# Kernel optimization log

Hardware: AMD Instinct MI355X
Metric: run time of the kernel (lower is better)

The kernel has to match this reference:

```python
import jax, jax.numpy as jnp
import numpy as np

B, N, D, C, ND = 32, 196, 512, 500, 51  # batch, patches, embed dim, classes, 1+50 descriptions


def _l2norm(x):
    return x / jnp.linalg.norm(x, axis=-1, keepdims=True)


def setup_inputs() -> dict:
    key = jax.random.key(0)
    k1, k2, k3, k4 = jax.random.split(key, 4)
    all_text = _l2norm(jax.random.normal(k3, (ND, C, D), jnp.float32))
    return {
        "image_features": _l2norm(jax.random.normal(k1, (B, D), jnp.float32)),
        "local_image_features": _l2norm(jax.random.normal(k2, (B, N, D), jnp.float32)),
        "all_text_features": all_text,
        "mean_text_features": _l2norm(jnp.mean(all_text, axis=0)),
        "topk": 50,
    }


def reference(image_features, local_image_features, all_text_features, mean_text_features, topk):
    # Faithful translation of get_dense_logits2 (m==1 global-feature axis squeezed out).
    base_logits = image_features @ mean_text_features.T                       # [B, C]
    # w[b,n] = <global image feat b, local patch feat n>
    w = jnp.einsum('bd,bnd->bn', image_features, local_image_features)        # [B, N]
    # v[nd,c]: softmax over descriptions of <mean text c, description nd of class c>
    v = jax.nn.softmax(
        jnp.einsum('cd,ncd->nc', mean_text_features, all_text_features), axis=0)  # [ND, C]
    # sim[b,c,nd,m] = <patch m of image b, description nd of class c>
    sim = jnp.einsum('bmd,ncd->bcnm', local_image_features, all_text_features)    # [B, C, ND, N]
    vals, idx = jax.lax.top_k(sim, topk)                                      # [B, C, ND, k] over patch axis
    sim_top = jnp.swapaxes(vals, 2, 3)                                        # [B, C, k, ND]
    # torch: idx[:, 0, :, 0] -> class 0, description 0, all k indices
    sel = idx[:, 0, 0, :]                                                     # [B, k]
    wg = jax.nn.softmax(jnp.take_along_axis(w, sel, axis=1), axis=-1)         # [B, k]
    # weight[b,c,m,n] = wg[b,m] * v[n,c]
    weight = wg[:, None, :, None] * jnp.swapaxes(v, 0, 1)[None, :, None, :]   # [B, C, k, ND]
    bias_logits = jnp.sum(sim_top * weight, axis=(-2, -1))                    # [B, C]
    return base_logits + bias_logits
```

## Files before the change

kernel.cpp:

```cpp
#include <hip/hip_runtime.h>

#define B_ 32
#define N_ 196
#define D_ 512
#define C_ 500
#define ND_ 51

typedef __attribute__((ext_vector_type(8))) short short8_t;
typedef __attribute__((ext_vector_type(4))) unsigned short us4_t;
typedef __attribute__((ext_vector_type(4))) float f32x4;

typedef const __attribute__((address_space(1))) unsigned int* gas_p;
typedef __attribute__((address_space(3))) unsigned int* las_p;
#define GLDS(gp, lp) __builtin_amdgcn_global_load_lds((gas_p)(gp), (las_p)(lp), 16, 0, 0)

__device__ inline unsigned short f2bf(float f) {
    unsigned u = __float_as_uint(f);
    u += 0x7FFFu + ((u >> 16) & 1u);
    return (unsigned short)(u >> 16);
}

template <int CTRL>
__device__ inline float dpp_mov(float x) {
    return __uint_as_float(__builtin_amdgcn_update_dpp(
        __float_as_uint(x), __float_as_uint(x), CTRL, 0xF, 0xF, true));
}
__device__ inline float rsum64(float v) {
    v += dpp_mov<0x121>(v);
    v += dpp_mov<0x122>(v);
    v += dpp_mov<0x124>(v);
    v += dpp_mov<0x128>(v);
    v += __shfl_xor(v, 16);
    v += __shfl_xor(v, 32);
    return v;
}
__device__ inline float rmax64(float v) {
    v = fmaxf(v, dpp_mov<0x121>(v));
    v = fmaxf(v, dpp_mov<0x122>(v));
    v = fmaxf(v, dpp_mov<0x124>(v));
    v = fmaxf(v, dpp_mov<0x128>(v));
    v = fmaxf(v, __shfl_xor(v, 16));
    v = fmaxf(v, __shfl_xor(v, 32));
    return v;
}
__device__ inline float rmin64(float v) {
    v = fminf(v, dpp_mov<0x121>(v));
    v = fminf(v, dpp_mov<0x122>(v));
    v = fminf(v, dpp_mov<0x124>(v));
    v = fminf(v, dpp_mov<0x128>(v));
    v = fminf(v, __shfl_xor(v, 16));
    v = fminf(v, __shfl_xor(v, 32));
    return v;
}
template <int S>
__device__ inline float xsh(float y) {
    if constexpr (S == 1) return dpp_mov<0xB1>(y);
    else if constexpr (S == 2) return dpp_mov<0x4E>(y);
    else if constexpr (S == 8) return dpp_mov<0x128>(y);
    else return __shfl_xor(y, S);
}

__global__ __launch_bounds__(256) void k_ctd(const float* __restrict__ text,
                                             const float* __restrict__ mean,
                                             unsigned short* __restrict__ textbf,
                                             float* __restrict__ dots) {
    const int row = blockIdx.x * 4 + (threadIdx.x >> 6);
    const int lane = threadIdx.x & 63;
    const int n = row / C_;
    const int ccol = row - n * C_;
    const float* tp = text + (size_t)row * 512 + lane * 8;
    const float* mp = mean + (size_t)ccol * 512 + lane * 8;
    const float4 f0 = *(const float4*)tp;
    const float4 f1 = *(const float4*)(tp + 4);
    const float4 m0 = *(const float4*)mp;
    const float4 m1 = *(const float4*)(mp + 4);
    float a = f0.x * m0.x + f0.y * m0.y + f0.z * m0.z + f0.w * m0.w
            + f1.x * m1.x + f1.y * m1.y + f1.z * m1.z + f1.w * m1.w;
    a = rsum64(a);
    const us4_t p0 = {f2bf(f0.x), f2bf(f0.y), f2bf(f0.z), f2bf(f0.w)};
    const us4_t p1 = {f2bf(f1.x), f2bf(f1.y), f2bf(f1.z), f2bf(f1.w)};
    *(us4_t*)&textbf[(size_t)row * 512 + lane * 8] = p0;
    *(us4_t*)&textbf[(size_t)row * 512 + lane * 8 + 4] = p1;
    if (lane == 0) dots[row] = a;
}

__global__ __launch_bounds__(64) void k_vsm(const float* __restrict__ dots,
                                            float* __restrict__ vout) {
    const int c = blockIdx.x;
    const int lane = threadIdx.x;
    float xv = (lane < ND_) ? dots[lane * C_ + c] : -INFINITY;
    float mx = rmax64(xv);
    float e = (lane < ND_) ? expf(xv - mx) : 0.f;
    float sum = rsum64(e);
    if (lane < ND_) vout[lane * C_ + c] = e / sum;
}

__global__ __launch_bounds__(256) void k_cls(const float* __restrict__ image,
                                             const float* __restrict__ localf,
                                             const float* __restrict__ text,
                                             unsigned short* __restrict__ localbf,
                                             float* __restrict__ s_ws,
                                             float* __restrict__ wm_ws) {
    const int row = blockIdx.x * 4 + (threadIdx.x >> 6);
    const int lane = threadIdx.x & 63;
    const int b = row / N_;
    const float* lp = localf + (size_t)row * 512 + lane * 8;
    const float4 l0 = *(const float4*)lp;
    const float4 l1 = *(const float4*)(lp + 4);
    const float* ip = image + b * 512 + lane * 8;
    const float* t0p = text + lane * 8;
    const float4 i0 = *(const float4*)ip, i1 = *(const float4*)(ip + 4);
    const float4 t0 = *(const float4*)t0p, t1 = *(const float4*)(t0p + 4);
    float a = l0.x * t0.x + l0.y * t0.y + l0.z * t0.z + l0.w * t0.w
            + l1.x * t1.x + l1.y * t1.y + l1.z * t1.z + l1.w * t1.w;
    float g = l0.x * i0.x + l0.y * i0.y + l0.z * i0.z + l0.w * i0.w
            + l1.x * i1.x + l1.y * i1.y + l1.z * i1.z + l1.w * i1.w;
    a = rsum64(a);
    g = rsum64(g);
    const us4_t p0 = {f2bf(l0.x), f2bf(l0.y), f2bf(l0.z), f2bf(l0.w)};
    const us4_t p1 = {f2bf(l1.x), f2bf(l1.y), f2bf(l1.z), f2bf(l1.w)};
    *(us4_t*)&localbf[(size_t)row * 512 + lane * 8] = p0;
    *(us4_t*)&localbf[(size_t)row * 512 + lane * 8 + 4] = p1;
    if (lane == 0) { s_ws[row] = a; wm_ws[row] = g; }
}

__global__ __launch_bounds__(256) void k_v(const float* __restrict__ mean,
                                           const float* __restrict__ text,
                                           float* __restrict__ vout) {
    const int c = blockIdx.x;
    const int w = threadIdx.x >> 6, lane = threadIdx.x & 63;
    __shared__ float sc[ND_];
    float md[8];
#pragma unroll
    for (int t = 0; t < 8; ++t) md[t] = mean[c * 512 + lane + 64 * t];
    for (int j = 0; j < 13; ++j) {
        const int n = w + 4 * j;
        if (n < ND_) {
            const float* tp = &text[((size_t)n * C_ + c) * 512];
            float a = 0.f;
#pragma unroll
            for (int t = 0; t < 8; ++t) a += md[t] * tp[lane + 64 * t];
            a = rsum64(a);
            if (lane == 0) sc[n] = a;
        }
    }
    __syncthreads();
    if (w == 0) {
        float xv = (lane < ND_) ? sc[lane] : -INFINITY;
        float mx = rmax64(xv);
        float e = (lane < ND_) ? expf(xv - mx) : 0.f;
        float sum = rsum64(e);
        if (lane < ND_) vout[lane * C_ + c] = e / sum;
    }
}

__global__ __launch_bounds__(256) void k_sw(const float* __restrict__ image,
                                            const float* __restrict__ localf,
                                            const float* __restrict__ text,
                                            float* __restrict__ s_ws,
                                            float* __restrict__ wm_ws) {
    const int b = blockIdx.x;
    const int m0 = blockIdx.y * 28;
    const int w = threadIdx.x >> 6, lane = threadIdx.x & 63;
    float t00[8], img[8];
#pragma unroll
    for (int t = 0; t < 8; ++t) {
        t00[t] = text[lane + 64 * t];
        img[t] = image[b * 512 + lane + 64 * t];
    }
    for (int t7 = 0; t7 < 7; ++t7) {
        const int m = m0 + w * 7 + t7;
        const float* lp = &localf[((size_t)b * N_ + m) * 512];
        float a = 0.f, g = 0.f;
#pragma unroll
        for (int t = 0; t < 8; ++t) {
            const float lv = lp[lane + 64 * t];
            a += t00[t] * lv;
            g += img[t] * lv;
        }
        a = rsum64(a);
        g = rsum64(g);
        if (lane == 0) { s_ws[b * N_ + m] = a; wm_ws[b * N_ + m] = g; }
    }
}

__global__ __launch_bounds__(64) void k_sel(const float* __restrict__ s_ws,
                                            const float* __restrict__ wm_ws,
                                            float* __restrict__ wgout) {
    const int b = blockIdx.x;
    const int lane = threadIdx.x;
    const unsigned long long ltmask = (1ull << lane) - 1ull;
    __shared__ float cv[64], cw[64];

    float x[4], p[4];
#pragma unroll
    for (int i = 0; i < 4; ++i) {
        const int m = lane + 64 * i;
        x[i] = (m < N_) ? s_ws[b * N_ + m] : -INFINITY;
        p[i] = (m < N_) ? wm_ws[b * N_ + m] : 0.f;
    }
    float lo = -1.02f, hi = 1.02f;
    int cl = N_;
    for (int it = 0; it < 24; ++it) {
        const float t = 0.5f * (lo + hi);
        int cnum = 0;
#pragma unroll
        for (int i = 0; i < 4; ++i) cnum += __popcll(__ballot(x[i] > t));
        if (cnum >= 50) { lo = t; cl = cnum; if (cnum <= 64) break; }
        else hi = t;
    }
    bool f[4];
    if (cl <= 64) {
#pragma unroll
        for (int i = 0; i < 4; ++i) f[i] = x[i] > lo;
    } else {
        int s1 = 0;
#pragma unroll
        for (int i = 0; i < 4; ++i) s1 += __popcll(__ballot(x[i] > hi));
        const int need = 64 - s1;
        int run = 0;
#pragma unroll
        for (int i = 0; i < 4; ++i) {
            const bool mid = (x[i] > lo) && !(x[i] > hi);
            const unsigned long long bm = __ballot(mid);
            const int pos = run + __popcll(bm & ltmask);
            f[i] = (x[i] > hi) || (mid && pos < need);
            run += __popcll(bm);
        }
    }
    int basep = 0;
#pragma unroll
    for (int i = 0; i < 4; ++i) {
        const unsigned long long bm = __ballot(f[i]);
        const int pos = basep + __popcll(bm & ltmask);
        if (f[i]) { cv[pos] = x[i]; cw[pos] = p[i]; }
        basep += __popcll(bm);
    }
    __builtin_amdgcn_s_waitcnt(0);
    float y = (lane < basep) ? cv[lane] : -INFINITY;
    float z = (lane < basep) ? cw[lane] : 0.f;
#pragma unroll
    for (int k = 2; k <= 64; k <<= 1) {
#pragma unroll
        for (int s2 = k >> 1; s2 > 0; s2 >>= 1) {
            const float py = __shfl_xor(y, s2);
            const float pz = __shfl_xor(z, s2);
            const bool keep_max = ((lane & k) == 0) == ((lane & s2) == 0);
            const bool take = keep_max ? (py > y) : (py < y);
            if (take) { y = py; z = pz; }
        }
    }
    float xv = (lane < 50) ? z : -INFINITY;
    float mx = xv;
#pragma unroll
    for (int off = 32; off; off >>= 1) mx = fmaxf(mx, __shfl_xor(mx, off));
    float e = (lane < 50) ? expf(xv - mx) : 0.f;
    float sum = e;
#pragma unroll
    for (int off = 32; off; off >>= 1) sum += __shfl_xor(sum, off);
    if (lane < 50) wgout[b * 50 + lane] = e / sum;
}

#define BSTEP(S, UP) { \
    const float q1 = xsh<S>(y1); \
    const float q2 = xsh<S>(y2); \
    if ((q1 > y1) == (UP)) y1 = q1; \
    if ((q2 > y2) == (UP)) y2 = q2; }

__global__ __launch_bounds__(512, 6) void k_main(const float* __restrict__ image,
                                                 const float* __restrict__ mean,
                                                 const unsigned short* __restrict__ localbf,
                                                 const unsigned short* __restrict__ textbf,
                                                 const float* __restrict__ vws,
                                                 const float* __restrict__ wgws,
                                                 float* __restrict__ out) {
    const int b = blockIdx.x;
    const int c = blockIdx.y;
    const int tid = threadIdx.x;
    const int w = tid >> 6;
    const int lane = tid & 63;
    const int quad = lane >> 4;
    const int l16 = lane & 15;

    __shared__ __align__(16) union SU {
        unsigned short stg[ND_ * 196 * 2];
        float ST[ND_ * 196];
    } u;

    float base_reg = 0.f;
    if (w == 0) {
        float s = 0.f;
#pragma unroll
        for (int t = 0; t < 8; ++t)
            s += image[b * 512 + lane + 64 * t] * mean[c * 512 + lane + 64 * t];
        s = rsum64(s);
        base_reg = s;
    }

    f32x4 acc[2][4];
    const f32x4 zv = {0.f, 0.f, 0.f, 0.f};
#pragma unroll
    for (int i = 0; i < 2; ++i)
#pragma unroll
        for (int j = 0; j < 4; ++j) acc[i][j] = zv;

    const unsigned short* abase = localbf + (size_t)(b * N_) * 512;

    const char* sp = (const char*)u.stg;
    const unsigned fb0 = (unsigned)(l16 * 128 + ((quad ^ (l16 & 7)) * 16));
    const unsigned fb1 = fb0 ^ 64u;
    const unsigned ab0 = fb0 + (unsigned)(w * 2048);
    const unsigned ab1 = fb1 + (unsigned)(w * 2048);

    for (int ks = 0; ks < 8; ++ks) {
#pragma unroll
        for (int i = 0; i < 4; ++i) {
            const int s = i * 512 + tid;
            if (s < 1568) {
                const int r = s >> 3;
                const int c8 = (s & 7) ^ (r & 7);
                GLDS(abase + (size_t)r * 512 + ks * 64 + c8 * 8, (char*)u.stg + s * 16);
            }
        }
        {
            const int s = tid;
            if (s < 408) {
                const int r = s >> 3;
                const int c8 = (s & 7) ^ (r & 7);
                GLDS(textbf + (size_t)(r * C_ + c) * 512 + ks * 64 + c8 * 8,
                     (char*)u.stg + 25088 + s * 16);
            }
        }
        __syncthreads();
#pragma unroll
        for (int kc = 0; kc < 2; ++kc) {
            const unsigned bb = kc ? fb1 : fb0;
            const unsigned aa = kc ? ab1 : ab0;
            short8_t bfr[4];
#pragma unroll
            for (int nt = 0; nt < 4; ++nt)
                bfr[nt] = *(const short8_t*)(sp + 25088 + bb + nt * 2048);
#pragma unroll
            for (int mi = 0; mi < 2; ++mi) {
                const int mt = w + 8 * mi;
                if (mt < 13) {
                    const short8_t af = *(const short8_t*)(sp + aa + mi * 16384);
#pragma unroll
                    for (int nt = 0; nt < 4; ++nt)
                        acc[mi][nt] = __builtin_amdgcn_mfma_f32_16x16x32_bf16(af, bfr[nt], acc[mi][nt], 0, 0, 0);
                }
            }
        }
        __syncthreads();
    }

#pragma unroll
    for (int nt = 0; nt < 4; ++nt) {
        const int n = nt * 16 + l16;
        if (n < ND_) {
#pragma unroll
            for (int mi = 0; mi < 2; ++mi) {
                const int mt = w + 8 * mi;
                if (mt < 12 || (mt == 12 && quad == 0))
                    *(f32x4*)&u.ST[n * 196 + mt * 16 + quad * 4] = acc[mi][nt];
            }
        }
    }
    __syncthreads();

    const float wgv = (lane < 50) ? wgws[b * 50 + lane] : 0.f;
    const unsigned long long ltmask = (1ull << lane) - 1ull;
    float waveacc = 0.f;

    const bool L0 = (lane & 1) == 0, L1 = (lane & 2) == 0, L2 = (lane & 4) == 0,
               L3 = (lane & 8) == 0, L4 = (lane & 16) == 0, L5 = (lane & 32) == 0;

    for (int t = 0; t < 4; ++t) {
        const int n1 = w + 16 * t;
        const int n2 = n1 + 8;
        const bool a2 = (n2 < ND_);
        if (n1 >= ND_) break;
        float* rowp1 = &u.ST[n1 * 196];
        float* rowp2 = &u.ST[(a2 ? n2 : n1) * 196];

        float x1[4], x2[4];
        float mn1 = INFINITY, mx1 = -INFINITY, mn2 = INFINITY, mx2 = -INFINITY;
        if (lane < 49) {
            f32x4 v1 = *(const f32x4*)&rowp1[lane * 4];
            f32x4 v2 = *(const f32x4*)&rowp2[lane * 4];
#pragma unroll
            for (int r = 0; r < 4; ++r) {
                x1[r] = v1[r];
                x2[r] = a2 ? v2[r] : -INFINITY;
                mx1 = fmaxf(mx1, x1[r]); mn1 = fminf(mn1, x1[r]);
                mx2 = fmaxf(mx2, x2[r]); mn2 = fminf(mn2, x2[r]);
            }
        } else {
#pragma unroll
            for (int r = 0; r < 4; ++r) { x1[r] = -INFINITY; x2[r] = -INFINITY; }
        }

        float hi1 = rmax64(mx1), lo1 = rmin64(mn1);
        float hi2 = rmax64(mx2), lo2 = rmin64(mn2);
        int cl1 = 256, cl2 = a2 ? 256 : 0;
        bool d1 = false, d2 = !a2;
        for (int it = 0; it < 24 && !(d1 && d2); ++it) {
            const float t1 = 0.5f * (lo1 + hi1);
            const float t2 = 0.5f * (lo2 + hi2);
            int cn1 = 0, cn2 = 0;
#pragma unroll
            for (int i = 0; i < 4; ++i) {
                cn1 += __popcll(__ballot(x1[i] > t1));
                cn2 += __popcll(__ballot(x2[i] > t2));
            }
            if (!d1) { if (cn1 >= 50) { lo1 = t1; cl1 = cn1; d1 = (cn1 <= 64); } else hi1 = t1; }
            if (!d2) { if (cn2 >= 50) { lo2 = t2; cl2 = cn2; d2 = (cn2 <= 64); } else hi2 = t2; }
        }

        bool f1[4], f2[4];
        int cnt1, cnt2;
        if (cl1 <= 64) {
#pragma unroll
            for (int i = 0; i < 4; ++i) f1[i] = x1[i] > lo1;
            cnt1 = cl1;
        } else {
            int s1 = 0;
#pragma unroll
            for (int i = 0; i < 4; ++i) s1 += __popcll(__ballot(x1[i] > hi1));
            const int need = 64 - s1;
            int run = 0;
#pragma unroll
            for (int i = 0; i < 4; ++i) {
                const bool mid = (x1[i] > lo1) && !(x1[i] > hi1);
                const unsigned long long bm = __ballot(mid);
                const int pos = run + __popcll(bm & ltmask);
                f1[i] = (x1[i] > hi1) || (mid && pos < need);
                run += __popcll(bm);
            }
            cnt1 = 64;
        }
        if (cl2 <= 64) {
#pragma unroll
            for (int i = 0; i < 4; ++i) f2[i] = x2[i] > lo2;
            cnt2 = cl2;
        } else {
            int s1 = 0;
#pragma unroll
            for (int i = 0; i < 4; ++i) s1 += __popcll(__ballot(x2[i] > hi2));
            const int need = 64 - s1;
            int run = 0;
#pragma unroll
            for (int i = 0; i < 4; ++i) {
                const bool mid = (x2[i] > lo2) && !(x2[i] > hi2);
                const unsigned long long bm = __ballot(mid);
                const int pos = run + __popcll(bm & ltmask);
                f2[i] = (x2[i] > hi2) || (mid && pos < need);
                run += __popcll(bm);
            }
            cnt2 = 64;
        }

        int bp1 = 0, bp2 = 0;
#pragma unroll
        for (int i = 0; i < 4; ++i) {
            const unsigned long long bm1 = __ballot(f1[i]);
            const unsigned long long bm2 = __ballot(f2[i]);
            const int p1 = bp1 + __popcll(bm1 & ltmask);
            const int p2 = bp2 + __popcll(bm2 & ltmask);
            if (f1[i]) rowp1[p1] = x1[i];
            if (f2[i]) rowp2[p2] = x2[i];
            bp1 += __popcll(bm1);
            bp2 += __popcll(bm2);
        }
        __builtin_amdgcn_s_waitcnt(0);
        float y1 = (lane < cnt1) ? rowp1[lane] : -INFINITY;
        float y2 = (lane < cnt2) ? rowp2[lane] : -INFINITY;

        BSTEP(1, L1 == L0)
        BSTEP(2, L2 == L1) BSTEP(1, L2 == L0)
        BSTEP(4, L3 == L2) BSTEP(2, L3 == L1) BSTEP(1, L3 == L0)
        BSTEP(8, L4 == L3) BSTEP(4, L4 == L2) BSTEP(2, L4 == L1) BSTEP(1, L4 == L0)
        BSTEP(16, L5 == L4) BSTEP(8, L5 == L3) BSTEP(4, L5 == L2) BSTEP(2, L5 == L1) BSTEP(1, L5 == L0)
        BSTEP(32, L5) BSTEP(16, L4) BSTEP(8, L3) BSTEP(4, L2) BSTEP(2, L1) BSTEP(1, L0)

        float part1 = (lane < 50) ? y1 * wgv : 0.f;
        float part2 = (lane < 50) ? y2 * wgv : 0.f;
        part1 = rsum64(part1);
        part2 = rsum64(part2);
        waveacc += vws[n1 * C_ + c] * part1;
        if (a2) waveacc += vws[n2 * C_ + c] * part2;
    }

    if (lane == 0) u.ST[w * 196] = waveacc;
    __syncthreads();
    if (tid == 0) {
        float r = base_reg;
#pragma unroll
        for (int i = 0; i < 8; ++i) r += u.ST[i * 196];
        out[b * C_ + c] = r;
    }
}

__global__ __launch_bounds__(256) void k_main_fb(const float* __restrict__ image,
                                                 const float* __restrict__ localf,
                                                 const float* __restrict__ text,
                                                 const float* __restrict__ mean,
                                                 const float* __restrict__ vws,
                                                 const float* __restrict__ wgws,
                                                 float* __restrict__ out) {
    const int c = blockIdx.x;
    const int b = blockIdx.y;
    const int tid = threadIdx.x;
    const int w = tid >> 6;
    const int lane = tid & 63;
    const int quad = lane >> 4;
    const int l16 = lane & 15;

    __shared__ __align__(16) union SU {
        struct { unsigned short A[208 * 72]; unsigned short Bm[64 * 72]; } st;
        float S[208 * 65];
    } u;
    __shared__ float wavepart[4];
    __shared__ float basev;

    if (w == 0) {
        float s = 0.f;
#pragma unroll
        for (int t = 0; t < 8; ++t)
            s += image[b * 512 + lane + 64 * t] * mean[c * 512 + lane + 64 * t];
#pragma unroll
        for (int off = 32; off; off >>= 1) s += __shfl_xor(s, off);
        if (lane == 0) basev = s;
    }

    f32x4 acc[4][4];
    const f32x4 zv = {0.f, 0.f, 0.f, 0.f};
#pragma unroll
    for (int i = 0; i < 4; ++i)
#pragma unroll
        for (int j = 0; j < 4; ++j) acc[i][j] = zv;

    const int lbase = (b * N_) * 512;
    for (int ks = 0; ks < 8; ++ks) {
        const int k0 = ks * 64;
        for (int e = tid; e < 3328; e += 256) {
            const int m = e >> 4, kc4 = e & 15;
            float4 fv = make_float4(0.f, 0.f, 0.f, 0.f);
            if (m < N_) fv = *(const float4*)&localf[lbase + m * 512 + k0 + kc4 * 4];
            us4_t pk = {f2bf(fv.x), f2bf(fv.y), f2bf(fv.z), f2bf(fv.w)};
            *(us4_t*)&u.st.A[m * 72 + kc4 * 4] = pk;
        }
        for (int e = tid; e < 1024; e += 256) {
            const int n = e >> 4, kc4 = e & 15;
            float4 fv = make_float4(0.f, 0.f, 0.f, 0.f);
            if (n < ND_) fv = *(const float4*)&text[((size_t)n * C_ + c) * 512 + k0 + kc4 * 4];
            us4_t pk = {f2bf(fv.x), f2bf(fv.y), f2bf(fv.z), f2bf(fv.w)};
            *(us4_t*)&u.st.Bm[n * 72 + kc4 * 4] = pk;
        }
        __syncthreads();
#pragma unroll
        for (int kc = 0; kc < 2; ++kc) {
            short8_t bfr[4];
#pragma unroll
            for (int nt = 0; nt < 4; ++nt)
                bfr[nt] = *(const short8_t*)&u.st.Bm[(nt * 16 + l16) * 72 + kc * 32 + quad * 8];
#pragma unroll
            for (int mi = 0; mi < 4; ++mi) {
                const int mt = w + 4 * mi;
                if (mt < 13) {
                    short8_t af = *(const short8_t*)&u.st.A[(mt * 16 + l16) * 72 + kc * 32 + quad * 8];
#pragma unroll
                    for (int nt = 0; nt < 4; ++nt)
                        acc[mi][nt] = __builtin_amdgcn_mfma_f32_16x16x32_bf16(af, bfr[nt], acc[mi][nt], 0, 0, 0);
                }
            }
        }
        __syncthreads();
    }

#pragma unroll
    for (int mi = 0; mi < 4; ++mi) {
        const int mt = w + 4 * mi;
        if (mt < 13) {
#pragma unroll
            for (int nt = 0; nt < 4; ++nt)
#pragma unroll
                for (int r = 0; r < 4; ++r)
                    u.S[(mt * 16 + quad * 4 + r) * 65 + nt * 16 + l16] = acc[mi][nt][r];
        }
    }
    __syncthreads();

    const float wgv = (lane < 50) ? wgws[b * 50 + lane] : 0.f;
    float waveacc = 0.f;

    for (int j = 0; j < 13; ++j) {
        const int n = w + 4 * j;
        if (n < ND_) {
            float x[4];
#pragma unroll
            for (int i = 0; i < 4; ++i) {
                const int m = lane + 64 * i;
                x[i] = (m < N_) ? u.S[m * 65 + n] : -INFINITY;
            }
#pragma unroll
            for (int k = 2; k <= 64; k <<= 1) {
#pragma unroll
                for (int s2 = k >> 1; s2 > 0; s2 >>= 1) {
                    const bool up = ((lane & k) == 0) == ((lane & s2) == 0);
#pragma unroll
                    for (int r = 0; r < 4; ++r) {
                        const float p = __shfl_xor(x[r], s2);
                        x[r] = up ? fmaxf(x[r], p) : fminf(x[r], p);
                    }
                }
            }
            float m01 = fmaxf(x[0], __shfl_xor(x[1], 63));
            float m23 = fmaxf(x[2], __shfl_xor(x[3], 63));
#pragma unroll
            for (int s2 = 32; s2 > 0; s2 >>= 1) {
                const bool up = (lane & s2) == 0;
                const float p0 = __shfl_xor(m01, s2);
                const float p1 = __shfl_xor(m23, s2);
                m01 = up ? fmaxf(m01, p0) : fminf(m01, p0);
                m23 = up ? fmaxf(m23, p1) : fminf(m23, p1);
            }
            float y = fmaxf(m01, __shfl_xor(m23, 63));
#pragma unroll
            for (int s2 = 32; s2 > 0; s2 >>= 1) {
                const bool up = (lane & s2) == 0;
                const float p = __shfl_xor(y, s2);
                y = up ? fmaxf(y, p) : fminf(y, p);
            }
            float part = (lane < 50) ? y * wgv : 0.f;
#pragma unroll
            for (int off = 32; off; off >>= 1) part += __shfl_xor(part, off);
            waveacc += vws[n * C_ + c] * part;
        }
    }

    if (lane == 0) wavepart[w] = waveacc;
    __syncthreads();
    if (tid == 0)
        out[b * C_ + c] = basev + wavepart[0] + wavepart[1] + wavepart[2] + wavepart[3];
}

extern "C" void kernel_launch(void* const* d_in, const int* in_sizes, int n_in,
                              void* d_out, int out_size, void* d_ws, size_t ws_size,
                              hipStream_t stream) {
    (void)in_sizes; (void)n_in; (void)out_size;
    const float* image = (const float*)d_in[0];
    const float* localf = (const float*)d_in[1];
    const float* text  = (const float*)d_in[2];
    const float* mean  = (const float*)d_in[3];
    float* out = (float*)d_out;

    float* vws   = (float*)d_ws;
    float* wgws  = vws + ND_ * C_;
    float* s_ws  = wgws + B_ * 50;
    float* wm_ws = s_ws + B_ * N_;
    float* dots  = wm_ws + B_ * N_;
    const size_t small_bytes = (size_t)(2 * ND_ * C_ + B_ * 50 + 2 * B_ * N_) * 4;
    const size_t bf_bytes = ((size_t)B_ * N_ * D_ + (size_t)ND_ * C_ * D_) * 2;

    if (ws_size >= small_bytes + bf_bytes) {
        unsigned short* localbf = (unsigned short*)(dots + ND_ * C_);
        unsigned short* textbf  = localbf + (size_t)B_ * N_ * D_;
        hipLaunchKernelGGL(k_ctd, dim3(ND_ * C_ / 4), dim3(256), 0, stream,
                           text, mean, textbf, dots);
        hipLaunchKernelGGL(k_vsm, dim3(C_), dim3(64), 0, stream, dots, vws);
        hipLaunchKernelGGL(k_cls, dim3(B_ * N_ / 4), dim3(256), 0, stream,
                           image, localf, text, localbf, s_ws, wm_ws);
        hipLaunchKernelGGL(k_sel, dim3(B_), dim3(64), 0, stream, s_ws, wm_ws, wgws);
        hipLaunchKernelGGL(k_main, dim3(B_, C_), dim3(512), 0, stream,
                           image, mean, localbf, textbf, vws, wgws, out);
    } else {
        hipLaunchKernelGGL(k_v, dim3(C_), dim3(256), 0, stream, mean, text, vws);
        hipLaunchKernelGGL(k_sw, dim3(B_, 7), dim3(256), 0, stream, image, localf, text, s_ws, wm_ws);
        hipLaunchKernelGGL(k_sel, dim3(B_), dim3(64), 0, stream, s_ws, wm_ws, wgws);
        hipLaunchKernelGGL(k_main_fb, dim3(C_, B_), dim3(256), 0, stream,
                           image, localf, text, mean, vws, wgws, out);
    }
}
```

Baseline: 622.3 us.

## Replace bisection-threshold top-k with bitonic sort and merge network

Replaces the per-row top-50 selection, which used iterative bisection on a threshold with ballots, compaction through LDS and a final 64-wide bitonic sort, with a branch-free bitonic network. Each of the four 64-element register columns is sorted, then pairs are merged by taking the max against the lane-reversed partner and re-running the bitonic merge, so the final register holds the top 64 in order. This removes the data-dependent loop iterations, ballots and LDS round-trip. In exchange it runs a fixed and larger number of DPP/shuffle compare-exchange steps per row.

```diff
diff --git a/kernel.cpp b/kernel.cpp
--- a/kernel.cpp
+++ b/kernel.cpp
@@ -41,15 +41,6 @@
     v = fmaxf(v, dpp_mov<0x128>(v));
     v = fmaxf(v, __shfl_xor(v, 16));
     v = fmaxf(v, __shfl_xor(v, 32));
-    return v;
-}
-__device__ inline float rmin64(float v) {
-    v = fminf(v, dpp_mov<0x121>(v));
-    v = fminf(v, dpp_mov<0x122>(v));
-    v = fminf(v, dpp_mov<0x124>(v));
-    v = fminf(v, dpp_mov<0x128>(v));
-    v = fminf(v, __shfl_xor(v, 16));
-    v = fminf(v, __shfl_xor(v, 32));
     return v;
 }
 template <int S>
@@ -261,11 +252,17 @@
     if (lane < 50) wgout[b * 50 + lane] = e / sum;
 }
 
-#define BSTEP(S, UP) { \
-    const float q1 = xsh<S>(y1); \
-    const float q2 = xsh<S>(y2); \
-    if ((q1 > y1) == (UP)) y1 = q1; \
-    if ((q2 > y2) == (UP)) y2 = q2; }
+#define BSTEP1(Y, S, UP) { const float q_ = xsh<S>(Y); if ((q_ > Y) == (UP)) Y = q_; }
+#define SORT64(Y) \
+    BSTEP1(Y, 1, L1 == L0) \
+    BSTEP1(Y, 2, L2 == L1) BSTEP1(Y, 1, L2 == L0) \
+    BSTEP1(Y, 4, L3 == L2) BSTEP1(Y, 2, L3 == L1) BSTEP1(Y, 1, L3 == L0) \
+    BSTEP1(Y, 8, L4 == L3) BSTEP1(Y, 4, L4 == L2) BSTEP1(Y, 2, L4 == L1) BSTEP1(Y, 1, L4 == L0) \
+    BSTEP1(Y, 16, L5 == L4) BSTEP1(Y, 8, L5 == L3) BSTEP1(Y, 4, L5 == L2) BSTEP1(Y, 2, L5 == L1) BSTEP1(Y, 1, L5 == L0) \
+    BSTEP1(Y, 32, L5) BSTEP1(Y, 16, L4) BSTEP1(Y, 8, L3) BSTEP1(Y, 4, L2) BSTEP1(Y, 2, L1) BSTEP1(Y, 1, L0)
+#define BSORT6(Y) \
+    BSTEP1(Y, 32, L5) BSTEP1(Y, 16, L4) BSTEP1(Y, 8, L3) BSTEP1(Y, 4, L2) BSTEP1(Y, 2, L1) BSTEP1(Y, 1, L0)
+#define MERGE2(A, B) { const float rb_ = __shfl_xor(B, 63); A = fmaxf(A, rb_); }
 
 __global__ __launch_bounds__(512, 6) void k_main(const float* __restrict__ image,
                                                  const float* __restrict__ mean,
@@ -369,7 +366,6 @@
     __syncthreads();
 
     const float wgv = (lane < 50) ? wgws[b * 50 + lane] : 0.f;
-    const unsigned long long ltmask = (1ull << lane) - 1ull;
     float waveacc = 0.f;
 
     const bool L0 = (lane & 1) == 0, L1 = (lane & 2) == 0, L2 = (lane & 4) == 0,
@@ -380,111 +376,32 @@
         const int n2 = n1 + 8;
         const bool a2 = (n2 < ND_);
         if (n1 >= ND_) break;
-        float* rowp1 = &u.ST[n1 * 196];
-        float* rowp2 = &u.ST[(a2 ? n2 : n1) * 196];
+        const float* rowp1 = &u.ST[n1 * 196];
+        const float* rowp2 = &u.ST[(a2 ? n2 : n1) * 196];
 
         float x1[4], x2[4];
-        float mn1 = INFINITY, mx1 = -INFINITY, mn2 = INFINITY, mx2 = -INFINITY;
         if (lane < 49) {
             f32x4 v1 = *(const f32x4*)&rowp1[lane * 4];
             f32x4 v2 = *(const f32x4*)&rowp2[lane * 4];
 #pragma unroll
-            for (int r = 0; r < 4; ++r) {
-                x1[r] = v1[r];
-                x2[r] = a2 ? v2[r] : -INFINITY;
-                mx1 = fmaxf(mx1, x1[r]); mn1 = fminf(mn1, x1[r]);
-                mx2 = fmaxf(mx2, x2[r]); mn2 = fminf(mn2, x2[r]);
-            }
+            for (int r = 0; r < 4; ++r) { x1[r] = v1[r]; x2[r] = a2 ? v2[r] : -INFINITY; }
         } else {
 #pragma unroll
             for (int r = 0; r < 4; ++r) { x1[r] = -INFINITY; x2[r] = -INFINITY; }
         }
 
-        float hi1 = rmax64(mx1), lo1 = rmin64(mn1);
-        float hi2 = rmax64(mx2), lo2 = rmin64(mn2);
-        int cl1 = 256, cl2 = a2 ? 256 : 0;
-        bool d1 = false, d2 = !a2;
-        for (int it = 0; it < 24 && !(d1 && d2); ++it) {
-            const float t1 = 0.5f * (lo1 + hi1);
-            const float t2 = 0.5f * (lo2 + hi2);
-            int cn1 = 0, cn2 = 0;
-#pragma unroll
-            for (int i = 0; i < 4; ++i) {
-                cn1 += __popcll(__ballot(x1[i] > t1));
-                cn2 += __popcll(__ballot(x2[i] > t2));
-            }
-            if (!d1) { if (cn1 >= 50) { lo1 = t1; cl1 = cn1; d1 = (cn1 <= 64); } else hi1 = t1; }
-            if (!d2) { if (cn2 >= 50) { lo2 = t2; cl2 = cn2; d2 = (cn2 <= 64); } else hi2 = t2; }
-        }
-
-        bool f1[4], f2[4];
-        int cnt1, cnt2;
-        if (cl1 <= 64) {
-#pragma unroll
-            for (int i = 0; i < 4; ++i) f1[i] = x1[i] > lo1;
-            cnt1 = cl1;
-        } else {
-            int s1 = 0;
-#pragma unroll
-            for (int i = 0; i < 4; ++i) s1 += __popcll(__ballot(x1[i] > hi1));
-            const int need = 64 - s1;
-            int run = 0;
-#pragma unroll
-            for (int i = 0; i < 4; ++i) {
-                const bool mid = (x1[i] > lo1) && !(x1[i] > hi1);
-                const unsigned long long bm = __ballot(mid);
-                const int pos = run + __popcll(bm & ltmask);
-                f1[i] = (x1[i] > hi1) || (mid && pos < need);
-                run += __popcll(bm);
-            }
-            cnt1 = 64;
-        }
-        if (cl2 <= 64) {
-#pragma unroll
-            for (int i = 0; i < 4; ++i) f2[i] = x2[i] > lo2;
-            cnt2 = cl2;
-        } else {
-            int s1 = 0;
-#pragma unroll
-            for (int i = 0; i < 4; ++i) s1 += __popcll(__ballot(x2[i] > hi2));
-            const int need = 64 - s1;
-            int run = 0;
-#pragma unroll
-            for (int i = 0; i < 4; ++i) {
-                const bool mid = (x2[i] > lo2) && !(x2[i] > hi2);
-                const unsigned long long bm = __ballot(mid);
-                const int pos = run + __popcll(bm & ltmask);
-                f2[i] = (x2[i] > hi2) || (mid && pos < need);
-                run += __popcll(bm);
-            }
-            cnt2 = 64;
-        }
-
-        int bp1 = 0, bp2 = 0;
-#pragma unroll
-        for (int i = 0; i < 4; ++i) {
-            const unsigned long long bm1 = __ballot(f1[i]);
-            const unsigned long long bm2 = __ballot(f2[i]);
-            const int p1 = bp1 + __popcll(bm1 & ltmask);
-            const int p2 = bp2 + __popcll(bm2 & ltmask);
-            if (f1[i]) rowp1[p1] = x1[i];
-            if (f2[i]) rowp2[p2] = x2[i];
-            bp1 += __popcll(bm1);
-            bp2 += __popcll(bm2);
-        }
-        __builtin_amdgcn_s_waitcnt(0);
-        float y1 = (lane < cnt1) ? rowp1[lane] : -INFINITY;
-        float y2 = (lane < cnt2) ? rowp2[lane] : -INFINITY;
-
-        BSTEP(1, L1 == L0)
-        BSTEP(2, L2 == L1) BSTEP(1, L2 == L0)
-        BSTEP(4, L3 == L2) BSTEP(2, L3 == L1) BSTEP(1, L3 == L0)
-        BSTEP(8, L4 == L3) BSTEP(4, L4 == L2) BSTEP(2, L4 == L1) BSTEP(1, L4 == L0)
-        BSTEP(16, L5 == L4) BSTEP(8, L5 == L3) BSTEP(4, L5 == L2) BSTEP(2, L5 == L1) BSTEP(1, L5 == L0)
-        BSTEP(32, L5) BSTEP(16, L4) BSTEP(8, L3) BSTEP(4, L2) BSTEP(2, L1) BSTEP(1, L0)
-
-        float part1 = (lane < 50) ? y1 * wgv : 0.f;
-        float part2 = (lane < 50) ? y2 * wgv : 0.f;
+#pragma unroll
+        for (int r = 0; r < 4; ++r) { SORT64(x1[r]) SORT64(x2[r]) }
+
+        MERGE2(x1[0], x1[1]) MERGE2(x1[2], x1[3])
+        MERGE2(x2[0], x2[1]) MERGE2(x2[2], x2[3])
+        BSORT6(x1[0]) BSORT6(x1[2]) BSORT6(x2[0]) BSORT6(x2[2])
+
+        MERGE2(x1[0], x1[2]) MERGE2(x2[0], x2[2])
+        BSORT6(x1[0]) BSORT6(x2[0])
+
+        float part1 = (lane < 50) ? x1[0] * wgv : 0.f;
+        float part2 = (lane < 50) ? x2[0] * wgv : 0.f;
         part1 = rsum64(part1);
         part2 = rsum64(part2);
         waveacc += vws[n1 * C_ + c] * part1;
```

Measured after the change: 837.2 us. 1.35x slower.
